# Optimization experiments

Hardware: AMD Instinct MI355X
Metric: run time of the kernel (lower is better)

## Reference

```python
import jax, jax.numpy as jnp
import numpy as np

B, T, E, H = 8, 1024, 128, 8
S = E // H  # 16, narrow per-head dim


def setup_inputs() -> dict:
    key = jax.random.key(0)
    ks = jax.random.split(key, 7)
    return {
        "x": jax.random.normal(ks[0], (B, T, E), dtype=jnp.float32),
        "masks": jax.random.randint(ks[1], (B, T), 0, 2, dtype=jnp.int32),
        "Wq": jax.random.normal(ks[2], (S, S), dtype=jnp.float32) * 0.05,
        "Wk": jax.random.normal(ks[3], (S, S), dtype=jnp.float32) * 0.05,
        "Wv": jax.random.normal(ks[4], (S, S), dtype=jnp.float32) * 0.05,
        "Wu": jax.random.normal(ks[5], (E, E), dtype=jnp.float32) * 0.05,
        "bu": jnp.zeros((E,), dtype=jnp.float32),
        "temporal_only": 1,
    }


def reference(x, masks, Wq, Wk, Wv, Wu, bu, temporal_only):
    b, t, e = x.shape
    h = H
    s = e // h
    x4 = x.reshape(b, t, h, s)
    # nn.Linear(s, s, bias=False): y = x @ W.T, applied per head
    q = jnp.einsum('bths,ds->bthd', x4, Wq)
    k = jnp.einsum('bths,ds->bthd', x4, Wk)
    v = jnp.einsum('bths,ds->bthd', x4, Wv)
    scale = jnp.float32(e) ** 0.25
    q = q / scale
    k = k / scale
    # (b, h, t, t) attention logits
    dot = jnp.einsum('bqhd,bkhd->bhqk', q, k)
    # temporal_only masking: masks is (b, t), applied on key axis then query axis
    m = masks.astype(bool)
    neg = jnp.float32(-1e9)
    dot = jnp.where(m[:, None, None, :], dot, neg)
    dot = jnp.where(m[:, None, :, None], dot, neg)
    attn = jax.nn.softmax(dot, axis=-1)
    # post-softmax zeroing with the same masks
    attn = jnp.where(m[:, None, None, :], attn, jnp.float32(0.0))
    attn = jnp.where(m[:, None, :, None], attn, jnp.float32(0.0))
    out = jnp.einsum('bhqk,bkhd->bqhd', attn, v).reshape(b, t, h * s)
    return out @ Wu.T + bu
```

## Files before the change

kernel.cpp:

```cpp
#include <hip/hip_runtime.h>

#define NB 8
#define NT 1024
#define NE 128
#define NH 8
#define NS 16

#define WS_Q 0
#define WS_K 1048576
#define WS_V 2097152
#define WS_Y 3145728
#define WS_VIDX 4194304

#define WT_PITCH 132

typedef float v2f __attribute__((ext_vector_type(2)));

static __device__ __forceinline__ v2f vlo(const float4 v) { return v2f{v.x, v.y}; }
static __device__ __forceinline__ v2f vhi(const float4 v) { return v2f{v.z, v.w}; }
static __device__ __forceinline__ v2f pfma(v2f a, v2f b, v2f c) {
  return __builtin_elementwise_fma(a, b, c);
}

static __device__ __forceinline__ void fma4(float4& acc, float s, const float4 v) {
  v2f lo = pfma(v2f{s, s}, vlo(v), vlo(acc));
  v2f hi = pfma(v2f{s, s}, vhi(v), vhi(acc));
  acc.x = lo.x; acc.y = lo.y; acc.z = hi.x; acc.w = hi.y;
}

static __device__ __forceinline__ float dot16p(const float4 q0, const float4 q1,
                                               const float4 q2, const float4 q3,
                                               const float4 k0, const float4 k1,
                                               const float4 k2, const float4 k3) {
  v2f a = vlo(q0) * vlo(k0);
  v2f b = vhi(q0) * vhi(k0);
  a = pfma(vlo(q1), vlo(k1), a);
  b = pfma(vhi(q1), vhi(k1), b);
  a = pfma(vlo(q2), vlo(k2), a);
  b = pfma(vhi(q2), vhi(k2), b);
  a = pfma(vlo(q3), vlo(k3), a);
  b = pfma(vhi(q3), vhi(k3), b);
  v2f c = a + b;
  return c.x + c.y;
}

__global__ __launch_bounds__(256) void qkv_kernel(
    const float* __restrict__ x, const int* __restrict__ masks,
    const float* __restrict__ Wq, const float* __restrict__ Wk,
    const float* __restrict__ Wv, float* __restrict__ Q, float* __restrict__ K,
    float* __restrict__ V, int* __restrict__ vidx, int* __restrict__ vcount) {
  if (blockIdx.x >= 1024) {
    const int b = blockIdx.x - 1024;
    const int lane = threadIdx.x;
    if (lane < 64) {
      int base = 0;
      for (int c = 0; c < NT; c += 64) {
        int t = c + lane;
        int v = masks[b * NT + t] != 0;
        unsigned long long bal = __ballot(v);
        int pos = base + __popcll(bal & ((1ull << lane) - 1ull));
        if (v) vidx[b * NT + pos] = t;
        base += __popcll(bal);
      }
      if (lane == 0) vcount[b] = base;
    }
    return;
  }
  const int tid = threadIdx.x;
  const int h = blockIdx.x & 7;
  const int rg = blockIdx.x >> 3;
  const int b = rg >> 4;
  const int base = rg << 6;
  const int d = tid & 15;
  const int r = base + ((tid >> 4) << 2);
  const float4* wq4 = (const float4*)(Wq + d * 16);
  const float4 wq0 = wq4[0], wq1 = wq4[1], wq2 = wq4[2], wq3 = wq4[3];
  const float4* wk4 = (const float4*)(Wk + d * 16);
  const float4 wk0 = wk4[0], wk1 = wk4[1], wk2 = wk4[2], wk3 = wk4[3];
  const float4* wv4 = (const float4*)(Wv + d * 16);
  const float4 wv0 = wv4[0], wv1 = wv4[1], wv2 = wv4[2], wv3 = wv4[3];
  const float invs = 0.08838834764831845f;
#pragma unroll
  for (int i = 0; i < 4; i++) {
    const int row = r + i;
    const float4* xp = (const float4*)(x + (size_t)row * 128 + h * 16);
    const float4 x0 = xp[0], x1 = xp[1], x2 = xp[2], x3 = xp[3];
    float aq = dot16p(x0, x1, x2, x3, wq0, wq1, wq2, wq3);
    float ak = dot16p(x0, x1, x2, x3, wk0, wk1, wk2, wk3);
    float av = dot16p(x0, x1, x2, x3, wv0, wv1, wv2, wv3);
    const int t = row & 1023;
    size_t o = ((size_t)(b * NH + h) * NT + t) * NS + d;
    Q[o] = aq * invs;
    K[o] = ak;
    V[o] = av;
  }
}

__global__ __launch_bounds__(512) void attn_kernel(
    const float* __restrict__ Q, const float* __restrict__ K,
    const float* __restrict__ V, const int* __restrict__ masks,
    const int* __restrict__ vidx, const int* __restrict__ vcount,
    float* __restrict__ Y) {
  __shared__ __align__(16) float om[8 * 64 * 20];
  const int tid = threadIdx.x;
  const int lane = tid & 63;
  const int s = tid >> 6;
  const int bh = blockIdx.x >> 2;
  const int b = bh >> 3, h = bh & 7;
  const int tbase = (blockIdx.x & 3) << 8;
  const int nv = __builtin_amdgcn_readfirstlane(vcount[b]);

  float4 q[4][4];
#pragma unroll
  for (int qq = 0; qq < 4; qq++) {
    const float4* qg =
        (const float4*)(Q + ((size_t)bh * NT + tbase + (qq << 6) + lane) * NS);
    q[qq][0] = qg[0]; q[qq][1] = qg[1]; q[qq][2] = qg[2]; q[qq][3] = qg[3];
  }
  v2f o[4][8];
  float m[4], l[4];
#pragma unroll
  for (int qq = 0; qq < 4; qq++) {
    m[qq] = -1e30f; l[qq] = 0.f;
#pragma unroll
    for (int k = 0; k < 8; k++) o[qq][k] = v2f{0.f, 0.f};
  }

  const int p0 = s + (lane << 3);
  const int idx0 = (p0 < nv) ? vidx[b * NT + p0] : 0;
  const int idx1 = (p0 + 512 < nv) ? vidx[b * NT + p0 + 512] : 0;
  const float* Kb = K + (size_t)bh * NT * NS;
  const float* Vb = V + (size_t)bh * NT * NS;

#pragma unroll 1
  for (int r0 = 0; s + (r0 << 3) < nv; r0 += 4) {
    float sc[4][4];
    int kks[4];
#pragma unroll
    for (int i = 0; i < 4; i++) {
      const int r = r0 + i;
      const int kk = (r < 64) ? __builtin_amdgcn_readlane(idx0, r)
                              : __builtin_amdgcn_readlane(idx1, r - 64);
      kks[i] = kk;
      const float4* kp = (const float4*)(Kb + (size_t)kk * NS);
      const float4 k0 = kp[0], k1 = kp[1], k2 = kp[2], k3 = kp[3];
#pragma unroll
      for (int qq = 0; qq < 4; qq++)
        sc[qq][i] = dot16p(q[qq][0], q[qq][1], q[qq][2], q[qq][3], k0, k1, k2, k3);
    }
#pragma unroll
    for (int i = 0; i < 4; i++)
      if (s + ((r0 + i) << 3) >= nv) {
        sc[0][i] = -1e30f; sc[1][i] = -1e30f;
        sc[2][i] = -1e30f; sc[3][i] = -1e30f;
      }
    float p[4][4];
#pragma unroll
    for (int qq = 0; qq < 4; qq++) {
      float mb = fmaxf(fmaxf(sc[qq][0], sc[qq][1]), fmaxf(sc[qq][2], sc[qq][3]));
      if (mb > m[qq]) {
        float al = __expf(m[qq] - mb);
        v2f al2 = {al, al};
        l[qq] *= al;
#pragma unroll
        for (int k = 0; k < 8; k++) o[qq][k] *= al2;
        m[qq] = mb;
      }
      p[qq][0] = __expf(sc[qq][0] - m[qq]);
      p[qq][1] = __expf(sc[qq][1] - m[qq]);
      p[qq][2] = __expf(sc[qq][2] - m[qq]);
      p[qq][3] = __expf(sc[qq][3] - m[qq]);
      l[qq] += (p[qq][0] + p[qq][1]) + (p[qq][2] + p[qq][3]);
    }
#pragma unroll
    for (int i = 0; i < 4; i++) {
      const float4* vp = (const float4*)(Vb + (size_t)kks[i] * NS);
      const float4 v0 = vp[0], v1 = vp[1], v2 = vp[2], v3 = vp[3];
#pragma unroll
      for (int qq = 0; qq < 4; qq++) {
        const v2f pq = {p[qq][i], p[qq][i]};
        o[qq][0] = pfma(pq, vlo(v0), o[qq][0]);
        o[qq][1] = pfma(pq, vhi(v0), o[qq][1]);
        o[qq][2] = pfma(pq, vlo(v1), o[qq][2]);
        o[qq][3] = pfma(pq, vhi(v1), o[qq][3]);
        o[qq][4] = pfma(pq, vlo(v2), o[qq][4]);
        o[qq][5] = pfma(pq, vhi(v2), o[qq][5]);
        o[qq][6] = pfma(pq, vlo(v3), o[qq][6]);
        o[qq][7] = pfma(pq, vhi(v3), o[qq][7]);
      }
    }
  }

#pragma unroll
  for (int ph = 0; ph < 4; ph++) {
    __syncthreads();
    {
      float* pa = om + (s * 64 + lane) * 20;
#pragma unroll
      for (int k = 0; k < 8; k++) *(v2f*)(pa + k * 2) = o[ph][k];
      pa[16] = m[ph];
      pa[17] = l[ph];
    }
    __syncthreads();
    {
      const int q8 = tid >> 3;
      const int sub = tid & 7;
      float ms[8], ls[8];
#pragma unroll
      for (int ss = 0; ss < 8; ss++) {
        const float* pp = om + (ss * 64 + q8) * 20;
        ms[ss] = pp[16];
        ls[ss] = pp[17];
      }
      float M = fmaxf(fmaxf(fmaxf(ms[0], ms[1]), fmaxf(ms[2], ms[3])),
                      fmaxf(fmaxf(ms[4], ms[5]), fmaxf(ms[6], ms[7])));
      float L = 0.f;
      v2f y = {0.f, 0.f};
#pragma unroll
      for (int ss = 0; ss < 8; ss++) {
        float f = __expf(ms[ss] - M);
        L = fmaf(f, ls[ss], L);
        v2f ov = *(const v2f*)(om + (ss * 64 + q8) * 20 + sub * 2);
        y = pfma(v2f{f, f}, ov, y);
      }
      const int tq = tbase + (ph << 6) + q8;
      const int qm = masks[b * NT + tq];
      const float inv = (qm != 0 && L > 0.f) ? (1.0f / L) : 0.f;
      y *= v2f{inv, inv};
      *(v2f*)(Y + ((size_t)b * NT + tq) * NE + h * NS + sub * 2) = y;
    }
  }
}

__global__ __launch_bounds__(256) void proj_kernel(
    const float* __restrict__ Y, const float* __restrict__ Wu,
    const float* __restrict__ bu, float* __restrict__ out) {
  __shared__ __align__(16) float Wt[64 * WT_PITCH];
  __shared__ __align__(16) float Yt[16 * 128];
  const int tid = threadIdx.x;
  const int r0 = blockIdx.x * 16;
  const float4* yg = (const float4*)(Y + (size_t)r0 * 128);
  float4* yt4 = (float4*)Yt;
  yt4[tid] = yg[tid];
  yt4[tid + 256] = yg[tid + 256];
  const int c0 = (tid & 31) << 2;
  const int rg = (tid >> 5) & 3;
  const int eh = tid >> 7;
  float4 acc0 = {0, 0, 0, 0}, acc1 = {0, 0, 0, 0}, acc2 = {0, 0, 0, 0},
         acc3 = {0, 0, 0, 0};
  for (int e0 = 0; e0 < 128; e0 += 64) {
    __syncthreads();
#pragma unroll
    for (int p = 0; p < 8; p++) {
      int idx = tid + p * 256;
      int c = idx >> 4;
      int es = (idx & 15) << 2;
      float4 w = *(const float4*)(Wu + c * 128 + e0 + es);
      Wt[(es + 0) * WT_PITCH + c] = w.x;
      Wt[(es + 1) * WT_PITCH + c] = w.y;
      Wt[(es + 2) * WT_PITCH + c] = w.z;
      Wt[(es + 3) * WT_PITCH + c] = w.w;
    }
    __syncthreads();
    const int eb = eh << 5;
    const float* y0 = Yt + (rg * 4 + 0) * 128 + e0 + eb;
    const float* y1 = Yt + (rg * 4 + 1) * 128 + e0 + eb;
    const float* y2 = Yt + (rg * 4 + 2) * 128 + e0 + eb;
    const float* y3 = Yt + (rg * 4 + 3) * 128 + e0 + eb;
#pragma unroll 4
    for (int e = 0; e < 32; e += 4) {
      const float* wb = Wt + (eb + e) * WT_PITCH + c0;
      float4 w0 = *(const float4*)(wb + 0 * WT_PITCH);
      float4 w1 = *(const float4*)(wb + 1 * WT_PITCH);
      float4 w2 = *(const float4*)(wb + 2 * WT_PITCH);
      float4 w3 = *(const float4*)(wb + 3 * WT_PITCH);
      float4 ya = *(const float4*)(y0 + e);
      float4 yb = *(const float4*)(y1 + e);
      float4 yc = *(const float4*)(y2 + e);
      float4 yd = *(const float4*)(y3 + e);
      fma4(acc0, ya.x, w0); fma4(acc0, ya.y, w1); fma4(acc0, ya.z, w2); fma4(acc0, ya.w, w3);
      fma4(acc1, yb.x, w0); fma4(acc1, yb.y, w1); fma4(acc1, yb.z, w2); fma4(acc1, yb.w, w3);
      fma4(acc2, yc.x, w0); fma4(acc2, yc.y, w1); fma4(acc2, yc.z, w2); fma4(acc2, yc.w, w3);
      fma4(acc3, yd.x, w0); fma4(acc3, yd.y, w1); fma4(acc3, yd.z, w2); fma4(acc3, yd.w, w3);
    }
  }
  __syncthreads();
  if (eh == 1) {
    float* p = Wt + (tid & 127) * 20;
    *(float4*)(p + 0) = acc0; *(float4*)(p + 4) = acc1;
    *(float4*)(p + 8) = acc2; *(float4*)(p + 12) = acc3;
  }
  __syncthreads();
  if (eh == 0) {
    const float* p = Wt + tid * 20;
    float4 b4 = *(const float4*)(bu + c0);
    float4 q0 = *(const float4*)(p + 0);
    float4 q1 = *(const float4*)(p + 4);
    float4 q2 = *(const float4*)(p + 8);
    float4 q3 = *(const float4*)(p + 12);
    acc0.x += q0.x + b4.x; acc0.y += q0.y + b4.y; acc0.z += q0.z + b4.z; acc0.w += q0.w + b4.w;
    acc1.x += q1.x + b4.x; acc1.y += q1.y + b4.y; acc1.z += q1.z + b4.z; acc1.w += q1.w + b4.w;
    acc2.x += q2.x + b4.x; acc2.y += q2.y + b4.y; acc2.z += q2.z + b4.z; acc2.w += q2.w + b4.w;
    acc3.x += q3.x + b4.x; acc3.y += q3.y + b4.y; acc3.z += q3.z + b4.z; acc3.w += q3.w + b4.w;
    *(float4*)(out + (size_t)(r0 + rg * 4 + 0) * 128 + c0) = acc0;
    *(float4*)(out + (size_t)(r0 + rg * 4 + 1) * 128 + c0) = acc1;
    *(float4*)(out + (size_t)(r0 + rg * 4 + 2) * 128 + c0) = acc2;
    *(float4*)(out + (size_t)(r0 + rg * 4 + 3) * 128 + c0) = acc3;
  }
}

extern "C" void kernel_launch(void* const* d_in, const int* in_sizes, int n_in,
                              void* d_out, int out_size, void* d_ws,
                              size_t ws_size, hipStream_t stream) {
  const float* x = (const float*)d_in[0];
  const int* masks = (const int*)d_in[1];
  const float* Wq = (const float*)d_in[2];
  const float* Wk = (const float*)d_in[3];
  const float* Wv = (const float*)d_in[4];
  const float* Wu = (const float*)d_in[5];
  const float* bu = (const float*)d_in[6];
  float* out = (float*)d_out;

  float* ws = (float*)d_ws;
  float* Q = ws + WS_Q;
  float* K = ws + WS_K;
  float* V = ws + WS_V;
  float* Y = ws + WS_Y;
  int* vidx = (int*)(ws + WS_VIDX);
  int* vcount = vidx + NB * NT;

  qkv_kernel<<<1024 + NB, 256, 0, stream>>>(x, masks, Wq, Wk, Wv, Q, K, V,
                                            vidx, vcount);
  attn_kernel<<<NB * NH * (NT / 256), 512, 0, stream>>>(Q, K, V, masks, vidx,
                                                        vcount, Y);
  proj_kernel<<<NB * NT / 16, 256, 0, stream>>>(Y, Wu, bu, out);
}
```

Measured before the change: 146.6 us.

## Stage gathered K/V tiles in shared memory and stage x rows in projection

The attention kernel now cooperatively gathers 128 valid keys' K and V rows into shared memory per tile, and each wave reads them from LDS instead of issuing scattered global loads indexed through readlane. The QKV projection kernel also loads its 64x16 x slice into shared memory once with coalesced float4 loads before computing. This is meant to cut redundant and uncoalesced global traffic, at the cost of extra __syncthreads per tile and a shared buffer reused for the reduction phase.

```diff
diff --git a/kernel.cpp b/kernel.cpp
--- a/kernel.cpp
+++ b/kernel.cpp
@@ -66,13 +66,19 @@
     }
     return;
   }
+  __shared__ __align__(16) float xs[64 * 20];
   const int tid = threadIdx.x;
   const int h = blockIdx.x & 7;
   const int rg = blockIdx.x >> 3;
   const int b = rg >> 4;
   const int base = rg << 6;
+  {
+    const int sr = tid >> 2, sq = tid & 3;
+    float4 xv = *(const float4*)(x + (size_t)(base + sr) * 128 + h * 16 + sq * 4);
+    *(float4*)(xs + sr * 20 + sq * 4) = xv;
+  }
   const int d = tid & 15;
-  const int r = base + ((tid >> 4) << 2);
+  const int r = (tid >> 4) << 2;
   const float4* wq4 = (const float4*)(Wq + d * 16);
   const float4 wq0 = wq4[0], wq1 = wq4[1], wq2 = wq4[2], wq3 = wq4[3];
   const float4* wk4 = (const float4*)(Wk + d * 16);
@@ -80,15 +86,16 @@
   const float4* wv4 = (const float4*)(Wv + d * 16);
   const float4 wv0 = wv4[0], wv1 = wv4[1], wv2 = wv4[2], wv3 = wv4[3];
   const float invs = 0.08838834764831845f;
+  __syncthreads();
 #pragma unroll
   for (int i = 0; i < 4; i++) {
     const int row = r + i;
-    const float4* xp = (const float4*)(x + (size_t)row * 128 + h * 16);
+    const float4* xp = (const float4*)(xs + row * 20);
     const float4 x0 = xp[0], x1 = xp[1], x2 = xp[2], x3 = xp[3];
     float aq = dot16p(x0, x1, x2, x3, wq0, wq1, wq2, wq3);
     float ak = dot16p(x0, x1, x2, x3, wk0, wk1, wk2, wk3);
     float av = dot16p(x0, x1, x2, x3, wv0, wv1, wv2, wv3);
-    const int t = row & 1023;
+    const int t = (base + row) & 1023;
     size_t o = ((size_t)(b * NH + h) * NT + t) * NS + d;
     Q[o] = aq * invs;
     K[o] = ak;
@@ -101,14 +108,16 @@
     const float* __restrict__ V, const int* __restrict__ masks,
     const int* __restrict__ vidx, const int* __restrict__ vcount,
     float* __restrict__ Y) {
-  __shared__ __align__(16) float om[8 * 64 * 20];
+  __shared__ __align__(16) float smem[10240];
+  float* Ks = smem;
+  float* Vs = smem + 2048;
   const int tid = threadIdx.x;
   const int lane = tid & 63;
   const int s = tid >> 6;
   const int bh = blockIdx.x >> 2;
   const int b = bh >> 3, h = bh & 7;
   const int tbase = (blockIdx.x & 3) << 8;
-  const int nv = __builtin_amdgcn_readfirstlane(vcount[b]);
+  const int nv = vcount[b];
 
   float4 q[4][4];
 #pragma unroll
@@ -126,71 +135,84 @@
     for (int k = 0; k < 8; k++) o[qq][k] = v2f{0.f, 0.f};
   }
 
-  const int p0 = s + (lane << 3);
-  const int idx0 = (p0 < nv) ? vidx[b * NT + p0] : 0;
-  const int idx1 = (p0 + 512 < nv) ? vidx[b * NT + p0 + 512] : 0;
-  const float* Kb = K + (size_t)bh * NT * NS;
-  const float* Vb = V + (size_t)bh * NT * NS;
-
-#pragma unroll 1
-  for (int r0 = 0; s + (r0 << 3) < nv; r0 += 4) {
-    float sc[4][4];
-    int kks[4];
-#pragma unroll
-    for (int i = 0; i < 4; i++) {
-      const int r = r0 + i;
-      const int kk = (r < 64) ? __builtin_amdgcn_readlane(idx0, r)
-                              : __builtin_amdgcn_readlane(idx1, r - 64);
-      kks[i] = kk;
-      const float4* kp = (const float4*)(Kb + (size_t)kk * NS);
-      const float4 k0 = kp[0], k1 = kp[1], k2 = kp[2], k3 = kp[3];
-#pragma unroll
-      for (int qq = 0; qq < 4; qq++)
-        sc[qq][i] = dot16p(q[qq][0], q[qq][1], q[qq][2], q[qq][3], k0, k1, k2, k3);
-    }
-#pragma unroll
-    for (int i = 0; i < 4; i++)
-      if (s + ((r0 + i) << 3) >= nv) {
-        sc[0][i] = -1e30f; sc[1][i] = -1e30f;
-        sc[2][i] = -1e30f; sc[3][i] = -1e30f;
-      }
-    float p[4][4];
-#pragma unroll
-    for (int qq = 0; qq < 4; qq++) {
-      float mb = fmaxf(fmaxf(sc[qq][0], sc[qq][1]), fmaxf(sc[qq][2], sc[qq][3]));
-      if (mb > m[qq]) {
-        float al = __expf(m[qq] - mb);
-        v2f al2 = {al, al};
-        l[qq] *= al;
-#pragma unroll
-        for (int k = 0; k < 8; k++) o[qq][k] *= al2;
-        m[qq] = mb;
-      }
-      p[qq][0] = __expf(sc[qq][0] - m[qq]);
-      p[qq][1] = __expf(sc[qq][1] - m[qq]);
-      p[qq][2] = __expf(sc[qq][2] - m[qq]);
-      p[qq][3] = __expf(sc[qq][3] - m[qq]);
-      l[qq] += (p[qq][0] + p[qq][1]) + (p[qq][2] + p[qq][3]);
-    }
-#pragma unroll
-    for (int i = 0; i < 4; i++) {
-      const float4* vp = (const float4*)(Vb + (size_t)kks[i] * NS);
-      const float4 v0 = vp[0], v1 = vp[1], v2 = vp[2], v3 = vp[3];
+  for (int k0 = 0; k0 < nv; k0 += 128) {
+    __syncthreads();
+    {
+      const int quad = tid & 3;
+      const int jr = tid >> 2;
+      int j = k0 + jr;
+      float4 kv = {0, 0, 0, 0}, vv = {0, 0, 0, 0};
+      if (j < nv) {
+        int kk = vidx[b * NT + j];
+        size_t bse = ((size_t)bh * NT + kk) * NS + (quad << 2);
+        kv = *(const float4*)(K + bse);
+        vv = *(const float4*)(V + bse);
+      }
+      *(float4*)(Ks + jr * 16 + (quad << 2)) = kv;
+      *(float4*)(Vs + jr * 16 + (quad << 2)) = vv;
+    }
+    __syncthreads();
+    int jmax = nv - k0;
+    if (jmax > 128) jmax = 128;
+    for (int g = 0; g < 4; g++) {
+      const int rb = s + (g << 5);
+      if (rb >= jmax) break;
+      float sc[4][4];
+#pragma unroll
+      for (int i = 0; i < 4; i++) {
+        const float4* kr = (const float4*)(Ks + (rb + (i << 3)) * 16);
+        const float4 k0v = kr[0], k1v = kr[1], k2v = kr[2], k3v = kr[3];
+#pragma unroll
+        for (int qq = 0; qq < 4; qq++)
+          sc[qq][i] =
+              dot16p(q[qq][0], q[qq][1], q[qq][2], q[qq][3], k0v, k1v, k2v, k3v);
+      }
+#pragma unroll
+      for (int i = 0; i < 4; i++)
+        if (rb + (i << 3) >= jmax) {
+          sc[0][i] = -1e30f; sc[1][i] = -1e30f;
+          sc[2][i] = -1e30f; sc[3][i] = -1e30f;
+        }
+      float p[4][4];
 #pragma unroll
       for (int qq = 0; qq < 4; qq++) {
-        const v2f pq = {p[qq][i], p[qq][i]};
-        o[qq][0] = pfma(pq, vlo(v0), o[qq][0]);
-        o[qq][1] = pfma(pq, vhi(v0), o[qq][1]);
-        o[qq][2] = pfma(pq, vlo(v1), o[qq][2]);
-        o[qq][3] = pfma(pq, vhi(v1), o[qq][3]);
-        o[qq][4] = pfma(pq, vlo(v2), o[qq][4]);
-        o[qq][5] = pfma(pq, vhi(v2), o[qq][5]);
-        o[qq][6] = pfma(pq, vlo(v3), o[qq][6]);
-        o[qq][7] = pfma(pq, vhi(v3), o[qq][7]);
-      }
-    }
-  }
-
+        float mb =
+            fmaxf(fmaxf(sc[qq][0], sc[qq][1]), fmaxf(sc[qq][2], sc[qq][3]));
+        if (mb > m[qq]) {
+          float al = __expf(m[qq] - mb);
+          v2f al2 = {al, al};
+          l[qq] *= al;
+#pragma unroll
+          for (int k = 0; k < 8; k++) o[qq][k] *= al2;
+          m[qq] = mb;
+        }
+        p[qq][0] = __expf(sc[qq][0] - m[qq]);
+        p[qq][1] = __expf(sc[qq][1] - m[qq]);
+        p[qq][2] = __expf(sc[qq][2] - m[qq]);
+        p[qq][3] = __expf(sc[qq][3] - m[qq]);
+        l[qq] += (p[qq][0] + p[qq][1]) + (p[qq][2] + p[qq][3]);
+      }
+#pragma unroll
+      for (int i = 0; i < 4; i++) {
+        const float4* vr = (const float4*)(Vs + (rb + (i << 3)) * 16);
+        const float4 v0 = vr[0], v1 = vr[1], v2 = vr[2], v3 = vr[3];
+#pragma unroll
+        for (int qq = 0; qq < 4; qq++) {
+          const v2f pq = {p[qq][i], p[qq][i]};
+          o[qq][0] = pfma(pq, vlo(v0), o[qq][0]);
+          o[qq][1] = pfma(pq, vhi(v0), o[qq][1]);
+          o[qq][2] = pfma(pq, vlo(v1), o[qq][2]);
+          o[qq][3] = pfma(pq, vhi(v1), o[qq][3]);
+          o[qq][4] = pfma(pq, vlo(v2), o[qq][4]);
+          o[qq][5] = pfma(pq, vhi(v2), o[qq][5]);
+          o[qq][6] = pfma(pq, vlo(v3), o[qq][6]);
+          o[qq][7] = pfma(pq, vhi(v3), o[qq][7]);
+        }
+      }
+    }
+  }
+
+  float* om = smem;
 #pragma unroll
   for (int ph = 0; ph < 4; ph++) {
     __syncthreads();
```

Result: faster. 135.6 us (-7.5%).
